# Optimization experiments

Hardware: AMD Instinct MI355X
Metric: run time of the kernel (lower is better)

## Reference

```python
import jax, jax.numpy as jnp
import numpy as np

B, S, D, H = 4, 2048, 1024, 16
HD = D // H  # head_dim = 64


def rope(x):
    # canonical interleaved RoPE over the full feature dim, applied pre-head-split
    # x: [B, S, D]
    d = x.shape[-1]
    inv_freq = 1.0 / (10000.0 ** (jnp.arange(0, d, 2, dtype=jnp.float32) / d))  # [D/2]
    pos = jnp.arange(x.shape[1], dtype=jnp.float32)
    ang = pos[:, None] * inv_freq[None, :]          # [S, D/2]
    cos, sin = jnp.cos(ang), jnp.sin(ang)
    x1, x2 = x[..., 0::2], x[..., 1::2]             # even/odd pairs
    r1 = x1 * cos - x2 * sin
    r2 = x1 * sin + x2 * cos
    return jnp.stack([r1, r2], axis=-1).reshape(x.shape)


def setup_inputs() -> dict:
    key = jax.random.key(0)
    ks = jax.random.split(key, 9)
    s = 1.0 / np.sqrt(D)
    def lin(k):
        kw, kb = jax.random.split(k)
        W = jax.random.uniform(kw, (D, D), jnp.float32, -s, s)
        b = jax.random.uniform(kb, (D,), jnp.float32, -s, s)
        return W, b
    Wq, bq = lin(ks[0]); Wk, bk = lin(ks[1]); Wv, bv = lin(ks[2]); W0, b0 = lin(ks[3])
    x = jax.random.normal(ks[4], (B, S, D), jnp.float32)
    return {"x": x, "Wq": Wq, "bq": bq, "Wk": Wk, "bk": bk,
            "Wv": Wv, "bv": bv, "W0": W0, "b0": b0}


def reference(x, Wq, bq, Wk, bk, Wv, bv, W0, b0):
    # QKV projections (torch Linear: x @ W.T + b; here W stored as [in, out])
    q = x @ Wq + bq
    k = x @ Wk + bk
    v = x @ Wv + bv
    # RoPE applied to full d_model before head split (as in the source)
    q = rope(q)
    k = rope(k)
    # split heads -> [B, H, S, HD]
    b, s, _ = x.shape
    qh = q.reshape(b, s, H, HD).transpose(0, 2, 1, 3)
    kh = k.reshape(b, s, H, HD).transpose(0, 2, 1, 3)
    vh = v.reshape(b, s, H, HD).transpose(0, 2, 1, 3)
    scores = jnp.einsum("bhqd,bhkd->bhqk", qh, kh) / jnp.sqrt(jnp.float32(HD))
    attn = jax.nn.softmax(scores, axis=-1)  # dropout p=0.0 -> identity
    out = jnp.einsum("bhqk,bhkd->bhqd", attn, vh)
    out = out.transpose(0, 2, 1, 3).reshape(b, s, D)
    return out @ W0 + b0
```

## Files before the change

kernel.cpp:

```cpp
#include <hip/hip_runtime.h>
#include <hip/hip_bf16.h>

typedef unsigned short u16;
typedef u16 u16x8 __attribute__((ext_vector_type(8)));
typedef u16 u16x4 __attribute__((ext_vector_type(4)));
typedef float f32x4 __attribute__((ext_vector_type(4)));
typedef __bf16 bf16x8 __attribute__((ext_vector_type(8)));

#define B_ 4
#define S_ 2048
#define D_ 1024
#define H_ 16
#define HD_ 64
#define M_ (B_*S_)

#if __has_builtin(__builtin_amdgcn_exp2f)
#define EXP2(x) __builtin_amdgcn_exp2f(x)
#else
#define EXP2(x) exp2f(x)
#endif

__device__ __forceinline__ f32x4 MFMA(u16x8 a, u16x8 b, f32x4 c) {
  return __builtin_amdgcn_mfma_f32_16x16x32_bf16(
      __builtin_bit_cast(bf16x8, a), __builtin_bit_cast(bf16x8, b), c, 0, 0, 0);
}

__device__ __forceinline__ u16 f2b(float f) {
  return __builtin_bit_cast(u16, __float2bfloat16(f));
}

__device__ __forceinline__ void load_lds16(const void* g, void* l) {
  __builtin_amdgcn_global_load_lds(
      (const __attribute__((address_space(1))) void*)g,
      (__attribute__((address_space(3))) void*)l, 16, 0, 0);
}

__device__ __forceinline__ unsigned int cvtpk(float lo, float hi) {
  unsigned int r;
  asm("v_cvt_pk_bf16_f32 %0, %1, %2" : "=v"(r) : "v"(lo), "v"(hi));
  return r;
}

__global__ __launch_bounds__(256) void k_rope_tab(float2* __restrict__ tab) {
  int i = blockIdx.x * 256 + threadIdx.x;
  if (i >= S_ * (D_ / 2)) return;
  int s = i >> 9;
  int f = i & 511;
  float invf = (float)exp(-(double)f / 512.0 * 9.210340371976184);
  float ang = (float)s * invf;
  tab[i] = make_float2(cosf(ang), sinf(ang));
}

__global__ __launch_bounds__(256) void k_cvt(const float* __restrict__ x,
                                             u16* __restrict__ xb, int n) {
  int i = blockIdx.x * 256 + threadIdx.x;
  if (i * 4 >= n) return;
  float4 v = ((const float4*)x)[i];
  ushort4 o;
  o.x = f2b(v.x); o.y = f2b(v.y); o.z = f2b(v.z); o.w = f2b(v.w);
  ((ushort4*)xb)[i] = o;
}

__global__ __launch_bounds__(256) void k_transpose(const float* __restrict__ W,
                                                   u16* __restrict__ WT) {
  __shared__ float t[32][33];
  int tx = threadIdx.x, ty = threadIdx.y;
  int bx = blockIdx.x * 32, by = blockIdx.y * 32;
#pragma unroll
  for (int j = 0; j < 32; j += 8)
    t[ty + j][tx] = W[(size_t)(by + ty + j) * D_ + bx + tx];
  __syncthreads();
#pragma unroll
  for (int j = 0; j < 32; j += 8)
    WT[(size_t)(bx + ty + j) * D_ + by + tx] = f2b(t[tx][ty + j]);
}

__global__ __launch_bounds__(256, 2) void k_gemm_qkv(
    const u16* __restrict__ A, const u16* __restrict__ WT3,
    const float* __restrict__ bq, const float* __restrict__ bk,
    const float* __restrict__ bv, const float2* __restrict__ tab,
    u16* __restrict__ Qh, u16* __restrict__ Kh, u16* __restrict__ Vt) {
  __shared__ __attribute__((aligned(16))) u16 Al[128 * 64];
  __shared__ __attribute__((aligned(16))) u16 Bl[128 * 64];
  const int tid = threadIdx.x;
  const int lane = tid & 63, wid = tid >> 6;
  const int wr = wid >> 1, wc = wid & 1;
  const int g = lane >> 4, c = lane & 15;
  const int flat = blockIdx.y * gridDim.x + blockIdx.x;
  const int xcd = flat & 7, idx = flat >> 3;
  const int bx = xcd * 8 + (idx & 7), by = idx >> 3;
  const int rowbase = bx * 128;
  const int colbaseG = by * 128;
  const int mode = by >> 3;
  const int colbase = colbaseG & 1023;

  f32x4 acc[4][4] = {};
  const int ldr = lane >> 3;
  const int ldk = (lane & 7) * 8;

  for (int kt = 0; kt < D_; kt += 64) {
    __syncthreads();
#pragma unroll
    for (int j = 0; j < 4; ++j) {
      const int chunk = wid * 4 + j;
      const int rr = chunk * 8 + ldr;
      load_lds16(A + (size_t)(rowbase + rr) * D_ + kt + ldk, &Al[chunk * 512]);
      load_lds16(WT3 + (size_t)(colbaseG + rr) * D_ + kt + ldk, &Bl[chunk * 512]);
    }
    __syncthreads();
#pragma unroll
    for (int ks = 0; ks < 2; ++ks) {
      u16x8 a[4], b[4];
#pragma unroll
      for (int m = 0; m < 4; ++m)
        a[m] = *(const u16x8*)&Al[(wr * 64 + m * 16 + c) * 64 + ks * 32 + g * 8];
#pragma unroll
      for (int n = 0; n < 4; ++n)
        b[n] = *(const u16x8*)&Bl[(wc * 64 + n * 16 + c) * 64 + ks * 32 + g * 8];
#pragma unroll
      for (int m = 0; m < 4; ++m)
#pragma unroll
        for (int n = 0; n < 4; ++n)
          acc[m][n] = MFMA(a[m], b[n], acc[m][n]);
    }
  }

  const float* bias = (mode == 0) ? bq : (mode == 1) ? bk : bv;
  u16* Cout = (mode == 0) ? Qh : (mode == 1) ? Kh : Vt;

  int coln[4];
  float bn[4];
#pragma unroll
  for (int n = 0; n < 4; ++n) {
    coln[n] = colbase + wc * 64 + n * 16 + c;
    bn[n] = bias[coln[n]];
  }

  if (mode == 2) {
#pragma unroll
    for (int m = 0; m < 4; ++m) {
      const int row0 = rowbase + wr * 64 + m * 16 + g * 4;
      const int s0 = row0 & (S_ - 1);
      const int bidx = row0 >> 11;
#pragma unroll
      for (int n = 0; n < 4; ++n) {
        const int h = coln[n] >> 6, hd = coln[n] & 63;
        ushort4 w;
        w.x = f2b(acc[m][n][0] + bn[n]);
        w.y = f2b(acc[m][n][1] + bn[n]);
        w.z = f2b(acc[m][n][2] + bn[n]);
        w.w = f2b(acc[m][n][3] + bn[n]);
        *(ushort4*)(Cout + ((size_t)(bidx * H_ + h) * HD_ + hd) * S_ + s0) = w;
      }
    }
  } else {
    const float qs = 0.18033688011112042f;
#pragma unroll
    for (int m = 0; m < 4; ++m) {
#pragma unroll
      for (int r = 0; r < 4; ++r) {
        const int row = rowbase + wr * 64 + m * 16 + g * 4 + r;
        const int s = row & (S_ - 1);
        const int bidx = row >> 11;
#pragma unroll
        for (int n = 0; n < 4; ++n) {
          float v = acc[m][n][r] + bn[n];
          float2 cs = tab[(size_t)s * 512 + (coln[n] >> 1)];
          float nb = __shfl_xor(v, 1);
          v = (lane & 1) ? (nb * cs.y + v * cs.x) : (v * cs.x - nb * cs.y);
          if (mode == 0) v *= qs;
          const int h = coln[n] >> 6, hd = coln[n] & 63;
          Cout[(((size_t)(bidx * H_ + h)) * S_ + s) * HD_ + hd] = f2b(v);
        }
      }
    }
  }
}

__global__ __launch_bounds__(256, 2) void k_gemm_o(
    const u16* __restrict__ A, const u16* __restrict__ BT,
    const float* __restrict__ bias, float* __restrict__ Cout) {
  __shared__ __attribute__((aligned(16))) u16 Al[128 * 64];
  __shared__ __attribute__((aligned(16))) u16 Bl[128 * 64];
  const int tid = threadIdx.x;
  const int lane = tid & 63, wid = tid >> 6;
  const int wr = wid >> 1, wc = wid & 1;
  const int g = lane >> 4, c = lane & 15;
  const int flat = blockIdx.y * gridDim.x + blockIdx.x;
  const int xcd = flat & 7, idx = flat >> 3;
  const int bx = xcd * 8 + (idx & 7), by = idx >> 3;
  const int rowbase = bx * 128, colbase = by * 128;

  f32x4 acc[4][4] = {};
  const int ldr = lane >> 3;
  const int ldk = (lane & 7) * 8;

  for (int kt = 0; kt < D_; kt += 64) {
    __syncthreads();
#pragma unroll
    for (int j = 0; j < 4; ++j) {
      const int chunk = wid * 4 + j;
      const int rr = chunk * 8 + ldr;
      load_lds16(A + (size_t)(rowbase + rr) * D_ + kt + ldk, &Al[chunk * 512]);
      load_lds16(BT + (size_t)(colbase + rr) * D_ + kt + ldk, &Bl[chunk * 512]);
    }
    __syncthreads();
#pragma unroll
    for (int ks = 0; ks < 2; ++ks) {
      u16x8 a[4], b[4];
#pragma unroll
      for (int m = 0; m < 4; ++m)
        a[m] = *(const u16x8*)&Al[(wr * 64 + m * 16 + c) * 64 + ks * 32 + g * 8];
#pragma unroll
      for (int n = 0; n < 4; ++n)
        b[n] = *(const u16x8*)&Bl[(wc * 64 + n * 16 + c) * 64 + ks * 32 + g * 8];
#pragma unroll
      for (int m = 0; m < 4; ++m)
#pragma unroll
        for (int n = 0; n < 4; ++n)
          acc[m][n] = MFMA(a[m], b[n], acc[m][n]);
    }
  }

  int coln[4];
  float bn[4];
#pragma unroll
  for (int n = 0; n < 4; ++n) {
    coln[n] = colbase + wc * 64 + n * 16 + c;
    bn[n] = bias[coln[n]];
  }
#pragma unroll
  for (int m = 0; m < 4; ++m)
#pragma unroll
    for (int r = 0; r < 4; ++r) {
      const int row = rowbase + wr * 64 + m * 16 + g * 4 + r;
#pragma unroll
      for (int n = 0; n < 4; ++n)
        Cout[(size_t)row * D_ + coln[n]] = acc[m][n][r] + bn[n];
    }
}

__global__ __launch_bounds__(256, 4) void k_attn(const u16* __restrict__ Qh,
                                                 const u16* __restrict__ Kh,
                                                 const u16* __restrict__ Vt,
                                                 u16* __restrict__ AO) {
  __shared__ __attribute__((aligned(16))) u16 Kl0[4096], Kl1[4096];
  __shared__ __attribute__((aligned(16))) u16 Vl0[4096], Vl1[4096];
  __shared__ __attribute__((aligned(16))) u16 Pl[4096];
  const int tid = threadIdx.x;
  const int lane = tid & 63, wid = tid >> 6;
  const int g = lane >> 4, c = lane & 15;
  const int flat = blockIdx.y * 32 + blockIdx.x;
  const int swzid = (flat & 7) * 256 + (flat >> 3);
  const int qt = swzid & 31, bh = swzid >> 5;
  const size_t base = (size_t)bh * S_ * HD_;
  const int qr0 = qt * 64 + wid * 16;

  u16x8 qf[2];
#pragma unroll
  for (int ks = 0; ks < 2; ++ks)
    qf[ks] = *(const u16x8*)(Qh + base + (size_t)(qr0 + c) * HD_ + ks * 32 + g * 8);

  f32x4 o2[4] = {};
  float L = 0.f;

  const int swz = (c & 7) << 3;
  const int kb0 = c * 64 + ((g * 8) ^ swz);
  const int kb1 = c * 64 + (((32 + g * 8)) ^ swz);
  const int pw0 = wid * 1024 + ((c * 64 + 0 * 16 + g * 4) ^ swz);
  const int pw1 = wid * 1024 + ((c * 64 + 1 * 16 + g * 4) ^ swz);
  const int pw2 = wid * 1024 + ((c * 64 + 2 * 16 + g * 4) ^ swz);
  const int pw3 = wid * 1024 + ((c * 64 + 3 * 16 + g * 4) ^ swz);
  const int pb0 = wid * 1024 + kb0;
  const int pb1 = wid * 1024 + kb1;
  const f32x4 z4 = {0.f, 0.f, 0.f, 0.f};

  const int ldrow = lane >> 3, ldslot = lane & 7;
  const int key0 = wid * 16 + ldrow, key1 = wid * 16 + 8 + ldrow;
  const u16* kp0 = Kh + base + (size_t)key0 * HD_ + (ldslot ^ (key0 & 7)) * 8;
  const u16* kp1 = Kh + base + (size_t)key1 * HD_ + (ldslot ^ (key1 & 7)) * 8;
  const u16* vp0 = Vt + base + (size_t)key0 * S_ + (ldslot ^ (key0 & 7)) * 8;
  const u16* vp1 = Vt + base + (size_t)key1 * S_ + (ldslot ^ (key1 & 7)) * 8;
  const int kdst0 = (wid * 16) * 64, kdst1 = (wid * 16 + 8) * 64;

#define STAGE(KP, VP)                                                        \
  {                                                                          \
    load_lds16(kp0, &KP[kdst0]); kp0 += 64 * HD_;                            \
    load_lds16(kp1, &KP[kdst1]); kp1 += 64 * HD_;                            \
    load_lds16(vp0, &VP[kdst0]); vp0 += 64;                                  \
    load_lds16(vp1, &VP[kdst1]); vp1 += 64;                                  \
  }

#define BODY(KC, VC, KP, VP)                                                 \
  {                                                                          \
    STAGE(KP, VP);                                                           \
    f32x4 s4[4];                                                             \
    __builtin_amdgcn_s_setprio(1);                                           \
    _Pragma("unroll") for (int n = 0; n < 4; ++n) {                          \
      u16x8 kfa = *(const u16x8*)&KC[n * 1024 + kb0];                        \
      u16x8 kfb = *(const u16x8*)&KC[n * 1024 + kb1];                        \
      s4[n] = MFMA(kfa, qf[0], z4);                                          \
      s4[n] = MFMA(kfb, qf[1], s4[n]);                                       \
    }                                                                        \
    __builtin_amdgcn_s_setprio(0);                                           \
    float p[4][4];                                                           \
    float rs = 0.f;                                                          \
    _Pragma("unroll") for (int n = 0; n < 4; ++n)                            \
        _Pragma("unroll") for (int r = 0; r < 4; ++r) {                      \
      p[n][r] = EXP2(s4[n][r]);                                              \
      rs += p[n][r];                                                         \
    }                                                                        \
    L += rs;                                                                 \
    {                                                                        \
      uint2 w0, w1, w2, w3;                                                  \
      w0.x = cvtpk(p[0][0], p[0][1]); w0.y = cvtpk(p[0][2], p[0][3]);        \
      w1.x = cvtpk(p[1][0], p[1][1]); w1.y = cvtpk(p[1][2], p[1][3]);        \
      w2.x = cvtpk(p[2][0], p[2][1]); w2.y = cvtpk(p[2][2], p[2][3]);        \
      w3.x = cvtpk(p[3][0], p[3][1]); w3.y = cvtpk(p[3][2], p[3][3]);        \
      *(uint2*)&Pl[pw0] = w0; *(uint2*)&Pl[pw1] = w1;                        \
      *(uint2*)&Pl[pw2] = w2; *(uint2*)&Pl[pw3] = w3;                        \
    }                                                                        \
    asm volatile("s_waitcnt lgkmcnt(0)" ::: "memory");                       \
    __builtin_amdgcn_sched_barrier(0);                                       \
    __builtin_amdgcn_s_setprio(1);                                           \
    {                                                                        \
      u16x8 pa0 = *(const u16x8*)&Pl[pb0];                                   \
      u16x8 pa1 = *(const u16x8*)&Pl[pb1];                                   \
      _Pragma("unroll") for (int nd = 0; nd < 4; ++nd) {                     \
        u16x8 va0 = *(const u16x8*)&VC[nd * 1024 + kb0];                     \
        u16x8 va1 = *(const u16x8*)&VC[nd * 1024 + kb1];                     \
        o2[nd] = MFMA(va0, pa0, o2[nd]);                                     \
        o2[nd] = MFMA(va1, pa1, o2[nd]);                                     \
      }                                                                      \
    }                                                                        \
    __builtin_amdgcn_s_setprio(0);                                           \
    __syncthreads();                                                         \
  }

  STAGE(Kl0, Vl0);
  __syncthreads();

#pragma unroll 1
  for (int it = 0; it < 16; ++it) {
    BODY(Kl0, Vl0, Kl1, Vl1);
    BODY(Kl1, Vl1, Kl0, Vl0);
  }

  L += __shfl_xor(L, 16);
  L += __shfl_xor(L, 32);
  const float inv = 1.f / L;
  const int b = bh >> 4, h = bh & (H_ - 1);
#pragma unroll
  for (int nd = 0; nd < 4; ++nd) {
    ushort4 w;
    w.x = f2b(o2[nd][0] * inv);
    w.y = f2b(o2[nd][1] * inv);
    w.z = f2b(o2[nd][2] * inv);
    w.w = f2b(o2[nd][3] * inv);
    *(ushort4*)(AO + ((size_t)(b * S_ + qr0 + c)) * D_ + h * HD_ + nd * 16 + g * 4) = w;
  }
#undef BODY
#undef STAGE
}

extern "C" void kernel_launch(void* const* d_in, const int* in_sizes, int n_in,
                              void* d_out, int out_size, void* d_ws,
                              size_t ws_size, hipStream_t stream) {
  const float* x  = (const float*)d_in[0];
  const float* Wq = (const float*)d_in[1];
  const float* bq = (const float*)d_in[2];
  const float* Wk = (const float*)d_in[3];
  const float* bk = (const float*)d_in[4];
  const float* Wv = (const float*)d_in[5];
  const float* bv = (const float*)d_in[6];
  const float* W0 = (const float*)d_in[7];
  const float* b0 = (const float*)d_in[8];
  float* out = (float*)d_out;

  char* ws = (char*)d_ws;
  const size_t MiB = (size_t)1 << 20;
  float2* tab = (float2*)(ws + 0);
  u16* xb  = (u16*)(ws + 8 * MiB);
  u16* WqT = (u16*)(ws + 24 * MiB);
  u16* WkT = (u16*)(ws + 26 * MiB);
  u16* WvT = (u16*)(ws + 28 * MiB);
  u16* W0T = (u16*)(ws + 30 * MiB);
  u16* Qh  = (u16*)(ws + 32 * MiB);
  u16* Kh  = (u16*)(ws + 48 * MiB);
  u16* Vt  = (u16*)(ws + 64 * MiB);
  u16* AO  = (u16*)(ws + 80 * MiB);

  k_rope_tab<<<4096, 256, 0, stream>>>(tab);
  k_cvt<<<(M_ * D_ / 4 + 255) / 256, 256, 0, stream>>>(x, xb, M_ * D_);
  {
    dim3 tb(32, 8), tg(32, 32);
    k_transpose<<<tg, tb, 0, stream>>>(Wq, WqT);
    k_transpose<<<tg, tb, 0, stream>>>(Wk, WkT);
    k_transpose<<<tg, tb, 0, stream>>>(Wv, WvT);
    k_transpose<<<tg, tb, 0, stream>>>(W0, W0T);
  }
  k_gemm_qkv<<<dim3(M_ / 128, 24), 256, 0, stream>>>(xb, WqT, bq, bk, bv, tab,
                                                     Qh, Kh, Vt);
  k_attn<<<dim3(S_ / 64, B_ * H_), 256, 0, stream>>>(Qh, Kh, Vt, AO);
  k_gemm_o<<<dim3(M_ / 128, D_ / 128), 256, 0, stream>>>(AO, W0T, b0, out);
}
```

Measured before the change: 216.5 us.

## Software-pipeline PV MFMA behind next QK, compute row sum via MFMA, merge transposes

The attention loop now preloads the V and P fragments into registers at the end of each iteration and issues the PV MFMAs together with the next tile's QK MFMAs, so matrix work overlaps the exp/convert phase. The softmax denominator is no longer summed with scalar adds and cross-lane shuffles. It is accumulated by an extra MFMA against a vector of bf16 ones, which means it is summed from the bf16-rounded probabilities. The four weight transpose launches are merged into one launch with a z-dimension selecting the matrix. Holding the prefetched fragments raises register pressure and may limit occupancy.

```diff
diff --git a/kernel.cpp b/kernel.cpp
--- a/kernel.cpp
+++ b/kernel.cpp
@@ -3,7 +3,6 @@
 
 typedef unsigned short u16;
 typedef u16 u16x8 __attribute__((ext_vector_type(8)));
-typedef u16 u16x4 __attribute__((ext_vector_type(4)));
 typedef float f32x4 __attribute__((ext_vector_type(4)));
 typedef __bf16 bf16x8 __attribute__((ext_vector_type(8)));
 
@@ -61,8 +60,15 @@
   ((ushort4*)xb)[i] = o;
 }
 
-__global__ __launch_bounds__(256) void k_transpose(const float* __restrict__ W,
-                                                   u16* __restrict__ WT) {
+__global__ __launch_bounds__(256) void k_transpose4(
+    const float* __restrict__ Wq, const float* __restrict__ Wk,
+    const float* __restrict__ Wv, const float* __restrict__ W0,
+    u16* __restrict__ Tq, u16* __restrict__ Tk, u16* __restrict__ Tv,
+    u16* __restrict__ T0) {
+  const float* W = (blockIdx.z == 0) ? Wq : (blockIdx.z == 1) ? Wk
+                   : (blockIdx.z == 2) ? Wv : W0;
+  u16* WT = (blockIdx.z == 0) ? Tq : (blockIdx.z == 1) ? Tk
+            : (blockIdx.z == 2) ? Tv : T0;
   __shared__ float t[32][33];
   int tx = threadIdx.x, ty = threadIdx.y;
   int bx = blockIdx.x * 32, by = blockIdx.y * 32;
@@ -262,11 +268,16 @@
     qf[ks] = *(const u16x8*)(Qh + base + (size_t)(qr0 + c) * HD_ + ks * 32 + g * 8);
 
   f32x4 o2[4] = {};
-  float L = 0.f;
+  f32x4 oL = {};
+  u16x8 vaP[8];
+  u16x8 paP0, paP1;
+  u16x8 onesf;
+#pragma unroll
+  for (int e = 0; e < 8; ++e) onesf[e] = 0x3F80;
 
   const int swz = (c & 7) << 3;
   const int kb0 = c * 64 + ((g * 8) ^ swz);
-  const int kb1 = c * 64 + (((32 + g * 8)) ^ swz);
+  const int kb1 = c * 64 + ((32 + g * 8) ^ swz);
   const int pw0 = wid * 1024 + ((c * 64 + 0 * 16 + g * 4) ^ swz);
   const int pw1 = wid * 1024 + ((c * 64 + 1 * 16 + g * 4) ^ swz);
   const int pw2 = wid * 1024 + ((c * 64 + 2 * 16 + g * 4) ^ swz);
@@ -291,7 +302,7 @@
     load_lds16(vp1, &VP[kdst1]); vp1 += 64;                                  \
   }
 
-#define BODY(KC, VC, KP, VP)                                                 \
+#define BODY(KC, VC, KP, VP, DOPV)                                           \
   {                                                                          \
     STAGE(KP, VP);                                                           \
     f32x4 s4[4];                                                             \
@@ -302,15 +313,19 @@
       s4[n] = MFMA(kfa, qf[0], z4);                                          \
       s4[n] = MFMA(kfb, qf[1], s4[n]);                                       \
     }                                                                        \
+    if (DOPV) {                                                              \
+      _Pragma("unroll") for (int nd = 0; nd < 4; ++nd) {                     \
+        o2[nd] = MFMA(vaP[nd * 2], paP0, o2[nd]);                            \
+        o2[nd] = MFMA(vaP[nd * 2 + 1], paP1, o2[nd]);                        \
+      }                                                                      \
+      oL = MFMA(onesf, paP0, oL);                                            \
+      oL = MFMA(onesf, paP1, oL);                                            \
+    }                                                                        \
     __builtin_amdgcn_s_setprio(0);                                           \
     float p[4][4];                                                           \
-    float rs = 0.f;                                                          \
     _Pragma("unroll") for (int n = 0; n < 4; ++n)                            \
-        _Pragma("unroll") for (int r = 0; r < 4; ++r) {                      \
+        _Pragma("unroll") for (int r = 0; r < 4; ++r)                        \
       p[n][r] = EXP2(s4[n][r]);                                              \
-      rs += p[n][r];                                                         \
-    }                                                                        \
-    L += rs;                                                                 \
     {                                                                        \
       uint2 w0, w1, w2, w3;                                                  \
       w0.x = cvtpk(p[0][0], p[0][1]); w0.y = cvtpk(p[0][2], p[0][3]);        \
@@ -322,33 +337,35 @@
     }                                                                        \
     asm volatile("s_waitcnt lgkmcnt(0)" ::: "memory");                       \
     __builtin_amdgcn_sched_barrier(0);                                       \
-    __builtin_amdgcn_s_setprio(1);                                           \
-    {                                                                        \
-      u16x8 pa0 = *(const u16x8*)&Pl[pb0];                                   \
-      u16x8 pa1 = *(const u16x8*)&Pl[pb1];                                   \
-      _Pragma("unroll") for (int nd = 0; nd < 4; ++nd) {                     \
-        u16x8 va0 = *(const u16x8*)&VC[nd * 1024 + kb0];                     \
-        u16x8 va1 = *(const u16x8*)&VC[nd * 1024 + kb1];                     \
-        o2[nd] = MFMA(va0, pa0, o2[nd]);                                     \
-        o2[nd] = MFMA(va1, pa1, o2[nd]);                                     \
-      }                                                                      \
+    _Pragma("unroll") for (int nd = 0; nd < 4; ++nd) {                       \
+      vaP[nd * 2] = *(const u16x8*)&VC[nd * 1024 + kb0];                     \
+      vaP[nd * 2 + 1] = *(const u16x8*)&VC[nd * 1024 + kb1];                 \
     }                                                                        \
-    __builtin_amdgcn_s_setprio(0);                                           \
+    paP0 = *(const u16x8*)&Pl[pb0];                                          \
+    paP1 = *(const u16x8*)&Pl[pb1];                                          \
     __syncthreads();                                                         \
   }
 
   STAGE(Kl0, Vl0);
   __syncthreads();
 
+  BODY(Kl0, Vl0, Kl1, Vl1, 0);
 #pragma unroll 1
-  for (int it = 0; it < 16; ++it) {
-    BODY(Kl0, Vl0, Kl1, Vl1);
-    BODY(Kl1, Vl1, Kl0, Vl0);
-  }
-
-  L += __shfl_xor(L, 16);
-  L += __shfl_xor(L, 32);
-  const float inv = 1.f / L;
+  for (int it = 0; it < 15; ++it) {
+    BODY(Kl1, Vl1, Kl0, Vl0, 1);
+    BODY(Kl0, Vl0, Kl1, Vl1, 1);
+  }
+  BODY(Kl1, Vl1, Kl0, Vl0, 1);
+
+#pragma unroll
+  for (int nd = 0; nd < 4; ++nd) {
+    o2[nd] = MFMA(vaP[nd * 2], paP0, o2[nd]);
+    o2[nd] = MFMA(vaP[nd * 2 + 1], paP1, o2[nd]);
+  }
+  oL = MFMA(onesf, paP0, oL);
+  oL = MFMA(onesf, paP1, oL);
+
+  const float inv = 1.f / oL[0];
   const int b = bh >> 4, h = bh & (H_ - 1);
 #pragma unroll
   for (int nd = 0; nd < 4; ++nd) {
@@ -392,13 +409,8 @@
 
   k_rope_tab<<<4096, 256, 0, stream>>>(tab);
   k_cvt<<<(M_ * D_ / 4 + 255) / 256, 256, 0, stream>>>(x, xb, M_ * D_);
-  {
-    dim3 tb(32, 8), tg(32, 32);
-    k_transpose<<<tg, tb, 0, stream>>>(Wq, WqT);
-    k_transpose<<<tg, tb, 0, stream>>>(Wk, WkT);
-    k_transpose<<<tg, tb, 0, stream>>>(Wv, WvT);
-    k_transpose<<<tg, tb, 0, stream>>>(W0, W0T);
-  }
+  k_transpose4<<<dim3(32, 32, 4), dim3(32, 8), 0, stream>>>(
+      Wq, Wk, Wv, W0, WqT, WkT, WvT, W0T);
   k_gemm_qkv<<<dim3(M_ / 128, 24), 256, 0, stream>>>(xb, WqT, bq, bk, bv, tab,
                                                      Qh, Kh, Vt);
   k_attn<<<dim3(S_ / 64, B_ * H_), 256, 0, stream>>>(Qh, Kh, Vt, AO);
```

Measured after the change: 217.4 us. No clear change (+0.4%).

## Replace 128x128 GEMMs with double-buffered 256x256 MFMA GEMM and merge weight transposes

Applied to the files above, without the earlier changes.

Both projection GEMMs are replaced by a single templated kernel with 256x256 output tiles, 512 threads, double-buffered LDS with XOR swizzling, interleaved async global-to-LDS loads, and s_setprio around MFMA bursts. This raises arithmetic intensity and overlaps loads with compute instead of fully serialising load and compute per K step. The four weight-transpose launches are merged into one launch via blockIdx.z. The trade-off is 128 KB of LDS per block and far fewer blocks (128 for the output GEMM), which may underfill the 256 CUs.

```diff
diff --git a/kernel.cpp b/kernel.cpp
--- a/kernel.cpp
+++ b/kernel.cpp
@@ -3,7 +3,6 @@
 
 typedef unsigned short u16;
 typedef u16 u16x8 __attribute__((ext_vector_type(8)));
-typedef u16 u16x4 __attribute__((ext_vector_type(4)));
 typedef float f32x4 __attribute__((ext_vector_type(4)));
 typedef __bf16 bf16x8 __attribute__((ext_vector_type(8)));
 
@@ -61,8 +60,15 @@
   ((ushort4*)xb)[i] = o;
 }
 
-__global__ __launch_bounds__(256) void k_transpose(const float* __restrict__ W,
-                                                   u16* __restrict__ WT) {
+__global__ __launch_bounds__(256) void k_transpose4(
+    const float* __restrict__ Wq, const float* __restrict__ Wk,
+    const float* __restrict__ Wv, const float* __restrict__ W0,
+    u16* __restrict__ Tq, u16* __restrict__ Tk, u16* __restrict__ Tv,
+    u16* __restrict__ T0) {
+  const float* W = (blockIdx.z == 0) ? Wq : (blockIdx.z == 1) ? Wk
+                   : (blockIdx.z == 2) ? Wv : W0;
+  u16* WT = (blockIdx.z == 0) ? Tq : (blockIdx.z == 1) ? Tk
+            : (blockIdx.z == 2) ? Tv : T0;
   __shared__ float t[32][33];
   int tx = threadIdx.x, ty = threadIdx.y;
   int bx = blockIdx.x * 32, by = blockIdx.y * 32;
@@ -75,169 +81,191 @@
     WT[(size_t)(bx + ty + j) * D_ + by + tx] = f2b(t[tx][ty + j]);
 }
 
-__global__ __launch_bounds__(256, 2) void k_gemm_qkv(
-    const u16* __restrict__ A, const u16* __restrict__ WT3,
-    const float* __restrict__ bq, const float* __restrict__ bk,
-    const float* __restrict__ bv, const float2* __restrict__ tab,
-    u16* __restrict__ Qh, u16* __restrict__ Kh, u16* __restrict__ Vt) {
-  __shared__ __attribute__((aligned(16))) u16 Al[128 * 64];
-  __shared__ __attribute__((aligned(16))) u16 Bl[128 * 64];
+template <int NM>
+__global__ __launch_bounds__(512, 2) void k_gemm256(
+    const u16* __restrict__ A, const u16* __restrict__ BT,
+    const float* __restrict__ b0p, const float* __restrict__ b1p,
+    const float* __restrict__ b2p, const float2* __restrict__ tab,
+    u16* __restrict__ O0, u16* __restrict__ O1, u16* __restrict__ O2,
+    float* __restrict__ FO) {
+  __shared__ __attribute__((aligned(16))) u16 Al0[16384], Al1[16384];
+  __shared__ __attribute__((aligned(16))) u16 Bl0[16384], Bl1[16384];
   const int tid = threadIdx.x;
   const int lane = tid & 63, wid = tid >> 6;
-  const int wr = wid >> 1, wc = wid & 1;
+  const int wm = wid >> 2, wn = wid & 3;
   const int g = lane >> 4, c = lane & 15;
-  const int flat = blockIdx.y * gridDim.x + blockIdx.x;
+  const int flat = blockIdx.x;
   const int xcd = flat & 7, idx = flat >> 3;
-  const int bx = xcd * 8 + (idx & 7), by = idx >> 3;
-  const int rowbase = bx * 128;
-  const int colbaseG = by * 128;
-  const int mode = by >> 3;
-  const int colbase = colbaseG & 1023;
-
-  f32x4 acc[4][4] = {};
-  const int ldr = lane >> 3;
-  const int ldk = (lane & 7) * 8;
-
-  for (int kt = 0; kt < D_; kt += 64) {
-    __syncthreads();
-#pragma unroll
-    for (int j = 0; j < 4; ++j) {
-      const int chunk = wid * 4 + j;
-      const int rr = chunk * 8 + ldr;
-      load_lds16(A + (size_t)(rowbase + rr) * D_ + kt + ldk, &Al[chunk * 512]);
-      load_lds16(WT3 + (size_t)(colbaseG + rr) * D_ + kt + ldk, &Bl[chunk * 512]);
+  const int bx = xcd * 4 + (idx & 3), by = idx >> 2;
+  const int rowbase = bx * 256;
+
+  const int rr_ = tid >> 3, slot = tid & 7;
+  const int sw8 = slot ^ (rr_ & 7);
+  const u16* aB = A + (size_t)(rowbase + rr_) * 1024 + sw8 * 8;
+  const u16* bB = BT + (size_t)(by * 256 + rr_) * 1024 + sw8 * 8;
+  const int wdst = wid * 512;
+
+  f32x4 acc[8][4] = {};
+  const int swz = (c & 7) << 3;
+  const int k0o = (g * 8) ^ swz;
+  const int k1o = k0o ^ 32;
+  const int ArdB = (wm * 128 + c) * 64;
+  const int BrdB = (wn * 64 + c) * 64;
+
+  u16x8 bf00, bf01, bf10, bf11, bf20, bf21, bf30, bf31;
+
+#define ISSUE_LO(NA, NB, KT)                                                 \
+  load_lds16(aB + (KT), &NA[wdst]);                                          \
+  load_lds16(aB + 65536 + (KT), &NA[4096 + wdst]);                           \
+  load_lds16(bB + (KT), &NB[wdst]);                                          \
+  load_lds16(bB + 65536 + (KT), &NB[4096 + wdst]);
+#define ISSUE_HI(NA, NB, KT)                                                 \
+  load_lds16(aB + 131072 + (KT), &NA[8192 + wdst]);                          \
+  load_lds16(aB + 196608 + (KT), &NA[12288 + wdst]);                         \
+  load_lds16(bB + 131072 + (KT), &NB[8192 + wdst]);                          \
+  load_lds16(bB + 196608 + (KT), &NB[12288 + wdst]);
+#define PBAR                                                                 \
+  __builtin_amdgcn_sched_barrier(0);                                         \
+  __builtin_amdgcn_s_barrier();                                              \
+  asm volatile("s_waitcnt lgkmcnt(0)" ::: "memory");                         \
+  __builtin_amdgcn_sched_barrier(0);                                         \
+  __builtin_amdgcn_s_setprio(1);
+#define PEND                                                                 \
+  __builtin_amdgcn_s_setprio(0);                                             \
+  __builtin_amdgcn_sched_barrier(0);                                         \
+  __builtin_amdgcn_s_barrier();
+#define LDB8(CB)                                                             \
+  bf00 = *(const u16x8*)&CB[BrdB + k0o];                                     \
+  bf01 = *(const u16x8*)&CB[BrdB + k1o];                                     \
+  bf10 = *(const u16x8*)&CB[BrdB + 1024 + k0o];                              \
+  bf11 = *(const u16x8*)&CB[BrdB + 1024 + k1o];                              \
+  bf20 = *(const u16x8*)&CB[BrdB + 2048 + k0o];                              \
+  bf21 = *(const u16x8*)&CB[BrdB + 2048 + k1o];                              \
+  bf30 = *(const u16x8*)&CB[BrdB + 3072 + k0o];                              \
+  bf31 = *(const u16x8*)&CB[BrdB + 3072 + k1o];
+#define LDA4(CA, MI0)                                                        \
+  a00 = *(const u16x8*)&CA[ArdB + (MI0) * 1024 + k0o];                       \
+  a01 = *(const u16x8*)&CA[ArdB + (MI0) * 1024 + k1o];                       \
+  a10 = *(const u16x8*)&CA[ArdB + (MI0 + 1) * 1024 + k0o];                   \
+  a11 = *(const u16x8*)&CA[ArdB + (MI0 + 1) * 1024 + k1o];
+#define MFMA16(MI0)                                                          \
+  acc[MI0][0] = MFMA(a00, bf00, acc[MI0][0]);                                \
+  acc[MI0][0] = MFMA(a01, bf01, acc[MI0][0]);                                \
+  acc[MI0][1] = MFMA(a00, bf10, acc[MI0][1]);                                \
+  acc[MI0][1] = MFMA(a01, bf11, acc[MI0][1]);                                \
+  acc[MI0][2] = MFMA(a00, bf20, acc[MI0][2]);                                \
+  acc[MI0][2] = MFMA(a01, bf21, acc[MI0][2]);                                \
+  acc[MI0][3] = MFMA(a00, bf30, acc[MI0][3]);                                \
+  acc[MI0][3] = MFMA(a01, bf31, acc[MI0][3]);                                \
+  acc[MI0 + 1][0] = MFMA(a10, bf00, acc[MI0 + 1][0]);                        \
+  acc[MI0 + 1][0] = MFMA(a11, bf01, acc[MI0 + 1][0]);                        \
+  acc[MI0 + 1][1] = MFMA(a10, bf10, acc[MI0 + 1][1]);                        \
+  acc[MI0 + 1][1] = MFMA(a11, bf11, acc[MI0 + 1][1]);                        \
+  acc[MI0 + 1][2] = MFMA(a10, bf20, acc[MI0 + 1][2]);                        \
+  acc[MI0 + 1][2] = MFMA(a11, bf21, acc[MI0 + 1][2]);                        \
+  acc[MI0 + 1][3] = MFMA(a10, bf30, acc[MI0 + 1][3]);                        \
+  acc[MI0 + 1][3] = MFMA(a11, bf31, acc[MI0 + 1][3]);
+#define TILE(CA, CB, NA, NB, KT, STG)                                        \
+  {                                                                          \
+    u16x8 a00, a01, a10, a11;                                                \
+    if (STG) { ISSUE_LO(NA, NB, KT) }                                        \
+    LDB8(CB) LDA4(CA, 0)                                                     \
+    PBAR MFMA16(0) PEND                                                      \
+    if (STG) { ISSUE_HI(NA, NB, KT) }                                        \
+    LDA4(CA, 2) PBAR MFMA16(2) PEND                                          \
+    LDA4(CA, 4) PBAR MFMA16(4) PEND                                          \
+    LDA4(CA, 6) PBAR MFMA16(6)                                               \
+    __builtin_amdgcn_s_setprio(0);                                           \
+    __syncthreads();                                                         \
+  }
+
+  ISSUE_LO(Al0, Bl0, 0)
+  ISSUE_HI(Al0, Bl0, 0)
+  __syncthreads();
+
+#pragma unroll 1
+  for (int it = 0; it < 7; ++it) {
+    const int kt1 = (2 * it + 1) * 64, kt2 = (2 * it + 2) * 64;
+    TILE(Al0, Bl0, Al1, Bl1, kt1, 1)
+    TILE(Al1, Bl1, Al0, Bl0, kt2, 1)
+  }
+  TILE(Al0, Bl0, Al1, Bl1, 15 * 64, 1)
+  TILE(Al1, Bl1, Al0, Bl0, 0, 0)
+
+  if (NM == 0) {
+    const int mode = by >> 2;
+    const float* bias = (mode == 0) ? b0p : (mode == 1) ? b1p : b2p;
+    u16* Cout = (mode == 0) ? O0 : (mode == 1) ? O1 : O2;
+    const int colL0 = (by & 3) * 256 + wn * 64;
+    int coln[4];
+    float bn[4];
+#pragma unroll
+    for (int ni = 0; ni < 4; ++ni) {
+      coln[ni] = colL0 + ni * 16 + c;
+      bn[ni] = bias[coln[ni]];
     }
-    __syncthreads();
-#pragma unroll
-    for (int ks = 0; ks < 2; ++ks) {
-      u16x8 a[4], b[4];
-#pragma unroll
-      for (int m = 0; m < 4; ++m)
-        a[m] = *(const u16x8*)&Al[(wr * 64 + m * 16 + c) * 64 + ks * 32 + g * 8];
-#pragma unroll
-      for (int n = 0; n < 4; ++n)
-        b[n] = *(const u16x8*)&Bl[(wc * 64 + n * 16 + c) * 64 + ks * 32 + g * 8];
-#pragma unroll
-      for (int m = 0; m < 4; ++m)
-#pragma unroll
-        for (int n = 0; n < 4; ++n)
-          acc[m][n] = MFMA(a[m], b[n], acc[m][n]);
-    }
-  }
-
-  const float* bias = (mode == 0) ? bq : (mode == 1) ? bk : bv;
-  u16* Cout = (mode == 0) ? Qh : (mode == 1) ? Kh : Vt;
-
-  int coln[4];
-  float bn[4];
-#pragma unroll
-  for (int n = 0; n < 4; ++n) {
-    coln[n] = colbase + wc * 64 + n * 16 + c;
-    bn[n] = bias[coln[n]];
-  }
-
-  if (mode == 2) {
-#pragma unroll
-    for (int m = 0; m < 4; ++m) {
-      const int row0 = rowbase + wr * 64 + m * 16 + g * 4;
-      const int s0 = row0 & (S_ - 1);
-      const int bidx = row0 >> 11;
-#pragma unroll
-      for (int n = 0; n < 4; ++n) {
-        const int h = coln[n] >> 6, hd = coln[n] & 63;
-        ushort4 w;
-        w.x = f2b(acc[m][n][0] + bn[n]);
-        w.y = f2b(acc[m][n][1] + bn[n]);
-        w.z = f2b(acc[m][n][2] + bn[n]);
-        w.w = f2b(acc[m][n][3] + bn[n]);
-        *(ushort4*)(Cout + ((size_t)(bidx * H_ + h) * HD_ + hd) * S_ + s0) = w;
+    if (mode == 2) {
+#pragma unroll
+      for (int mi = 0; mi < 8; ++mi) {
+        const int row0 = rowbase + wm * 128 + mi * 16 + g * 4;
+        const int s0 = row0 & (S_ - 1);
+        const int bidx = row0 >> 11;
+#pragma unroll
+        for (int ni = 0; ni < 4; ++ni) {
+          const int h = coln[ni] >> 6, hd = coln[ni] & 63;
+          ushort4 w;
+          w.x = f2b(acc[mi][ni][0] + bn[ni]);
+          w.y = f2b(acc[mi][ni][1] + bn[ni]);
+          w.z = f2b(acc[mi][ni][2] + bn[ni]);
+          w.w = f2b(acc[mi][ni][3] + bn[ni]);
+          *(ushort4*)(Cout + ((size_t)(bidx * H_ + h) * HD_ + hd) * S_ + s0) = w;
+        }
+      }
+    } else {
+      const float qs = 0.18033688011112042f;
+#pragma unroll
+      for (int mi = 0; mi < 8; ++mi) {
+#pragma unroll
+        for (int rq = 0; rq < 4; ++rq) {
+          const int row = rowbase + wm * 128 + mi * 16 + g * 4 + rq;
+          const int s = row & (S_ - 1);
+          const int bidx = row >> 11;
+#pragma unroll
+          for (int ni = 0; ni < 4; ++ni) {
+            float v = acc[mi][ni][rq] + bn[ni];
+            float2 cs = tab[(size_t)s * 512 + (coln[ni] >> 1)];
+            float nb = __shfl_xor(v, 1);
+            v = (lane & 1) ? (nb * cs.y + v * cs.x) : (v * cs.x - nb * cs.y);
+            if (mode == 0) v *= qs;
+            const int h = coln[ni] >> 6, hd = coln[ni] & 63;
+            Cout[(((size_t)(bidx * H_ + h)) * S_ + s) * HD_ + hd] = f2b(v);
+          }
+        }
       }
     }
   } else {
-    const float qs = 0.18033688011112042f;
-#pragma unroll
-    for (int m = 0; m < 4; ++m) {
-#pragma unroll
-      for (int r = 0; r < 4; ++r) {
-        const int row = rowbase + wr * 64 + m * 16 + g * 4 + r;
-        const int s = row & (S_ - 1);
-        const int bidx = row >> 11;
-#pragma unroll
-        for (int n = 0; n < 4; ++n) {
-          float v = acc[m][n][r] + bn[n];
-          float2 cs = tab[(size_t)s * 512 + (coln[n] >> 1)];
-          float nb = __shfl_xor(v, 1);
-          v = (lane & 1) ? (nb * cs.y + v * cs.x) : (v * cs.x - nb * cs.y);
-          if (mode == 0) v *= qs;
-          const int h = coln[n] >> 6, hd = coln[n] & 63;
-          Cout[(((size_t)(bidx * H_ + h)) * S_ + s) * HD_ + hd] = f2b(v);
+    const int colb = by * 256 + wn * 64;
+#pragma unroll
+    for (int mi = 0; mi < 8; ++mi) {
+#pragma unroll
+      for (int rq = 0; rq < 4; ++rq) {
+        const int row = rowbase + wm * 128 + mi * 16 + g * 4 + rq;
+#pragma unroll
+        for (int ni = 0; ni < 4; ++ni) {
+          const int coln = colb + ni * 16 + c;
+          FO[(size_t)row * D_ + coln] = acc[mi][ni][rq] + b0p[coln];
         }
       }
     }
   }
-}
-
-__global__ __launch_bounds__(256, 2) void k_gemm_o(
-    const u16* __restrict__ A, const u16* __restrict__ BT,
-    const float* __restrict__ bias, float* __restrict__ Cout) {
-  __shared__ __attribute__((aligned(16))) u16 Al[128 * 64];
-  __shared__ __attribute__((aligned(16))) u16 Bl[128 * 64];
-  const int tid = threadIdx.x;
-  const int lane = tid & 63, wid = tid >> 6;
-  const int wr = wid >> 1, wc = wid & 1;
-  const int g = lane >> 4, c = lane & 15;
-  const int flat = blockIdx.y * gridDim.x + blockIdx.x;
-  const int xcd = flat & 7, idx = flat >> 3;
-  const int bx = xcd * 8 + (idx & 7), by = idx >> 3;
-  const int rowbase = bx * 128, colbase = by * 128;
-
-  f32x4 acc[4][4] = {};
-  const int ldr = lane >> 3;
-  const int ldk = (lane & 7) * 8;
-
-  for (int kt = 0; kt < D_; kt += 64) {
-    __syncthreads();
-#pragma unroll
-    for (int j = 0; j < 4; ++j) {
-      const int chunk = wid * 4 + j;
-      const int rr = chunk * 8 + ldr;
-      load_lds16(A + (size_t)(rowbase + rr) * D_ + kt + ldk, &Al[chunk * 512]);
-      load_lds16(BT + (size_t)(colbase + rr) * D_ + kt + ldk, &Bl[chunk * 512]);
-    }
-    __syncthreads();
-#pragma unroll
-    for (int ks = 0; ks < 2; ++ks) {
-      u16x8 a[4], b[4];
-#pragma unroll
-      for (int m = 0; m < 4; ++m)
-        a[m] = *(const u16x8*)&Al[(wr * 64 + m * 16 + c) * 64 + ks * 32 + g * 8];
-#pragma unroll
-      for (int n = 0; n < 4; ++n)
-        b[n] = *(const u16x8*)&Bl[(wc * 64 + n * 16 + c) * 64 + ks * 32 + g * 8];
-#pragma unroll
-      for (int m = 0; m < 4; ++m)
-#pragma unroll
-        for (int n = 0; n < 4; ++n)
-          acc[m][n] = MFMA(a[m], b[n], acc[m][n]);
-    }
-  }
-
-  int coln[4];
-  float bn[4];
-#pragma unroll
-  for (int n = 0; n < 4; ++n) {
-    coln[n] = colbase + wc * 64 + n * 16 + c;
-    bn[n] = bias[coln[n]];
-  }
-#pragma unroll
-  for (int m = 0; m < 4; ++m)
-#pragma unroll
-    for (int r = 0; r < 4; ++r) {
-      const int row = rowbase + wr * 64 + m * 16 + g * 4 + r;
-#pragma unroll
-      for (int n = 0; n < 4; ++n)
-        Cout[(size_t)row * D_ + coln[n]] = acc[m][n][r] + bn[n];
-    }
+#undef TILE
+#undef MFMA16
+#undef LDA4
+#undef LDB8
+#undef PEND
+#undef PBAR
+#undef ISSUE_HI
+#undef ISSUE_LO
 }
 
 __global__ __launch_bounds__(256, 4) void k_attn(const u16* __restrict__ Qh,
@@ -266,7 +294,7 @@
 
   const int swz = (c & 7) << 3;
   const int kb0 = c * 64 + ((g * 8) ^ swz);
-  const int kb1 = c * 64 + (((32 + g * 8)) ^ swz);
+  const int kb1 = c * 64 + ((32 + g * 8) ^ swz);
   const int pw0 = wid * 1024 + ((c * 64 + 0 * 16 + g * 4) ^ swz);
   const int pw1 = wid * 1024 + ((c * 64 + 1 * 16 + g * 4) ^ swz);
   const int pw2 = wid * 1024 + ((c * 64 + 2 * 16 + g * 4) ^ swz);
@@ -392,15 +420,11 @@
 
   k_rope_tab<<<4096, 256, 0, stream>>>(tab);
   k_cvt<<<(M_ * D_ / 4 + 255) / 256, 256, 0, stream>>>(x, xb, M_ * D_);
-  {
-    dim3 tb(32, 8), tg(32, 32);
-    k_transpose<<<tg, tb, 0, stream>>>(Wq, WqT);
-    k_transpose<<<tg, tb, 0, stream>>>(Wk, WkT);
-    k_transpose<<<tg, tb, 0, stream>>>(Wv, WvT);
-    k_transpose<<<tg, tb, 0, stream>>>(W0, W0T);
-  }
-  k_gemm_qkv<<<dim3(M_ / 128, 24), 256, 0, stream>>>(xb, WqT, bq, bk, bv, tab,
-                                                     Qh, Kh, Vt);
+  k_transpose4<<<dim3(32, 32, 4), dim3(32, 8), 0, stream>>>(
+      Wq, Wk, Wv, W0, WqT, WkT, WvT, W0T);
+  k_gemm256<0><<<384, 512, 0, stream>>>(xb, WqT, bq, bk, bv, tab,
+                                        Qh, Kh, Vt, nullptr);
   k_attn<<<dim3(S_ / 64, B_ * H_), 256, 0, stream>>>(Qh, Kh, Vt, AO);
-  k_gemm_o<<<dim3(M_ / 128, D_ / 128), 256, 0, stream>>>(AO, W0T, b0, out);
-}
+  k_gemm256<1><<<128, 512, 0, stream>>>(AO, W0T, b0, nullptr, nullptr, nullptr,
+                                        nullptr, nullptr, nullptr, out);
+}
```

Result: no change. 214.2 us (-1.1%).
